# Performance work log

Hardware: AMD Instinct MI355X
Metric: run time of the kernel (lower is better)

## Reference

```python
import jax, jax.numpy as jnp
import numpy as np

VOCAB, EMB, HID = 256, 32, 128
B, T = 512, 512


def setup_inputs() -> dict:
    key = jax.random.key(0)
    ks = jax.random.split(key, 8)
    s_emb = 1.0  # torch nn.Embedding default N(0,1)
    s_lstm = 1.0 / np.sqrt(HID)  # torch LSTM uniform(-1/sqrt(H), 1/sqrt(H))
    s_cls = 1.0 / np.sqrt(HID)
    return {
        "inputs": jax.random.randint(ks[0], (B, T), 0, VOCAB, dtype=jnp.int64),
        "emb": jax.random.normal(ks[1], (VOCAB, EMB), jnp.float32) * s_emb,
        "W_ih": jax.random.uniform(ks[2], (4 * HID, EMB), jnp.float32, -s_lstm, s_lstm),
        "W_hh": jax.random.uniform(ks[3], (4 * HID, HID), jnp.float32, -s_lstm, s_lstm),
        "b_ih": jax.random.uniform(ks[4], (4 * HID,), jnp.float32, -s_lstm, s_lstm),
        "b_hh": jax.random.uniform(ks[5], (4 * HID,), jnp.float32, -s_lstm, s_lstm),
        "W_cls": jax.random.uniform(ks[6], (VOCAB, HID), jnp.float32, -s_cls, s_cls),
        "b_cls": jax.random.uniform(ks[7], (VOCAB,), jnp.float32, -s_cls, s_cls),
    }


def reference(inputs, emb, W_ih, W_hh, b_ih, b_hh, W_cls, b_cls):
    x = emb[inputs]  # [B, T, E]
    H = W_hh.shape[1]
    # Precompute input projections for all timesteps (batched GEMM): [B, T, 4H]
    xw = jnp.einsum("bte,ge->btg", x, W_ih) + b_ih + b_hh
    xw_t = jnp.transpose(xw, (1, 0, 2))  # [T, B, 4H]

    def step(carry, xw_step):
        h, c = carry
        gates = xw_step + h @ W_hh.T  # [B, 4H]
        i, f, g, o = jnp.split(gates, 4, axis=-1)  # torch gate order: i, f, g, o
        i = jax.nn.sigmoid(i)
        f = jax.nn.sigmoid(f)
        g = jnp.tanh(g)
        o = jax.nn.sigmoid(o)
        c = f * c + i * g
        h = o * jnp.tanh(c)
        return (h, c), None

    h0 = jnp.zeros((x.shape[0], H), x.dtype)
    c0 = jnp.zeros((x.shape[0], H), x.dtype)
    (h_last, _), _ = jax.lax.scan(step, (h0, c0), xw_t)
    # classifier on last hidden state: [B, vocab]
    return h_last @ W_cls.T + b_cls
```

## Files before the change

kernel.cpp:

```cpp
#include <hip/hip_runtime.h>
#include <hip/hip_bf16.h>

#define VOCAB 256
#define EMB   32
#define HID   128
#define GATES 512
#define BATCH 512
#define SEQ   512

typedef __attribute__((ext_vector_type(8))) short bf16x8;
typedef __attribute__((ext_vector_type(4))) float f32x4;

static __device__ __forceinline__ unsigned short f2bf(float f) {
  unsigned int u = __float_as_uint(f);
  return (unsigned short)((u + 0x7fffu + ((u >> 16) & 1u)) >> 16);
}

__global__ __launch_bounds__(256) void prep_kernel(
    const float* __restrict__ emb, const float* __restrict__ W_ih,
    const float* __restrict__ W_hh, const float* __restrict__ b_ih,
    const float* __restrict__ b_hh, float* __restrict__ P,
    unsigned short* __restrict__ Whh_bf) {
  const int wg  = blockIdx.x;
  const int tid = threadIdx.x;
  if (wg < VOCAB) {
    __shared__ float e[EMB];
    if (tid < EMB) e[tid] = emb[wg * EMB + tid];
    __syncthreads();
    for (int g = tid; g < GATES; g += 256) {
      float acc = b_ih[g] + b_hh[g];
      const float* w = W_ih + g * EMB;
      #pragma unroll
      for (int k = 0; k < EMB; ++k) acc += e[k] * w[k];
      P[wg * GATES + g] = acc;
    }
  } else {
    const int base = (wg - VOCAB) * 1024 + tid * 4;
    const float4 v = *(const float4*)(W_hh + base);
    ushort4 o;
    o.x = f2bf(v.x); o.y = f2bf(v.y); o.z = f2bf(v.z); o.w = f2bf(v.w);
    *(ushort4*)(Whh_bf + base) = o;
  }
}

__global__ __launch_bounds__(256, 1) void lstm_kernel(
    const int* __restrict__ inputs, const float* __restrict__ P,
    const unsigned short* __restrict__ Whh_bf,
    const float* __restrict__ W_cls, const float* __restrict__ b_cls,
    float* __restrict__ out) {
  const int wg   = blockIdx.x;
  const int tid  = threadIdx.x;
  const int wave = tid >> 6;
  const int lane = tid & 63;
  const int c16  = lane & 15;
  const int kg   = lane >> 4;
  const int b0   = wg * 2;

  const int row   = kg >> 1;
  const int jh    = kg & 1;
  const int jfull = wave * 32 + jh * 16 + c16;

  __shared__ unsigned char  chars[2][SEQ];
  __shared__ unsigned short hbuf[2][2][HID];
  __shared__ float          h_last[2][HID];

  for (int k = tid; k < 2 * SEQ; k += 256) {
    const int r = k >> 9, t = k & (SEQ - 1);
    chars[r][t] = (unsigned char)(inputs[(b0 + r) * SEQ + t] & 0xff);
  }
  ((unsigned short*)hbuf)[tid] = 0;

  bf16x8 Bfrag[8][4];
  #pragma unroll
  for (int gt = 0; gt < 4; ++gt)
    #pragma unroll
    for (int jhu = 0; jhu < 2; ++jhu) {
      const int g = gt * 128 + wave * 32 + jhu * 16 + c16;
      #pragma unroll
      for (int ks = 0; ks < 4; ++ks)
        Bfrag[gt * 2 + jhu][ks] = *(const bf16x8*)(Whh_bf + g * HID + ks * 32 + kg * 8);
    }

  const int aoff = (c16 & 1) * HID + kg * 8;
  const float* Pj = P + jfull;
  float cstate = 0.f;

  __syncthreads();

  #pragma unroll 1
  for (int t = 0; t < SEQ; ++t) {
    const int rb = t & 1;
    const int ch = chars[row][t];
    const float* Pr = Pj + ch * GATES;
    const float p0 = Pr[0];
    const float p1 = Pr[128];
    const float p2 = Pr[256];
    const float p3 = Pr[384];

    const unsigned short* hb = &hbuf[rb][0][0] + aoff;
    f32x4 acc[8] = {};
    #pragma unroll
    for (int ks = 0; ks < 4; ++ks) {
      const bf16x8 A = *(const bf16x8*)(hb + ks * 32);
      #pragma unroll
      for (int u = 0; u < 8; ++u)
        acc[u] = __builtin_amdgcn_mfma_f32_16x16x32_bf16(A, Bfrag[u][ks], acc[u], 0, 0, 0);
    }

    const float gi = jh ? (row ? acc[1][1] : acc[1][0]) : (row ? acc[0][1] : acc[0][0]);
    const float gf = jh ? (row ? acc[3][1] : acc[3][0]) : (row ? acc[2][1] : acc[2][0]);
    const float gg = jh ? (row ? acc[5][1] : acc[5][0]) : (row ? acc[4][1] : acc[4][0]);
    const float go = jh ? (row ? acc[7][1] : acc[7][0]) : (row ? acc[6][1] : acc[6][0]);

    const float ip = gi + p0;
    const float fp = gf + p1;
    const float gp = gg + p2;
    const float op = go + p3;
    const float iv = 1.f / (1.f + __expf(-ip));
    const float fv = 1.f / (1.f + __expf(-fp));
    const float gv = 1.f - 2.f / (__expf(2.f * gp) + 1.f);
    const float ov = 1.f / (1.f + __expf(-op));
    cstate = fv * cstate + iv * gv;
    const float th = 1.f - 2.f / (__expf(2.f * cstate) + 1.f);
    const float hv = ov * th;

    hbuf[rb ^ 1][row][jfull] = f2bf(hv);
    if (t == SEQ - 1) h_last[row][jfull] = hv;
    __syncthreads();
  }

  const int erow = tid >> 7;
  const int ej   = tid & 127;
  #pragma unroll
  for (int half = 0; half < 2; ++half) {
    const int v = ej + half * 128;
    float acc = b_cls[v];
    const float4* w  = (const float4*)(W_cls + v * HID);
    const float4* hh = (const float4*)&h_last[erow][0];
    #pragma unroll
    for (int k = 0; k < HID / 4; ++k) {
      const float4 wv = w[k];
      const float4 hv4 = hh[k];
      acc += wv.x * hv4.x + wv.y * hv4.y + wv.z * hv4.z + wv.w * hv4.w;
    }
    out[(b0 + erow) * VOCAB + v] = acc;
  }
}

extern "C" void kernel_launch(void* const* d_in, const int* in_sizes, int n_in,
                              void* d_out, int out_size, void* d_ws, size_t ws_size,
                              hipStream_t stream) {
  const int*   inputs = (const int*)d_in[0];
  const float* emb    = (const float*)d_in[1];
  const float* W_ih   = (const float*)d_in[2];
  const float* W_hh   = (const float*)d_in[3];
  const float* b_ih   = (const float*)d_in[4];
  const float* b_hh   = (const float*)d_in[5];
  const float* W_cls  = (const float*)d_in[6];
  const float* b_cls  = (const float*)d_in[7];
  float* outp = (float*)d_out;

  float* Ptab = (float*)d_ws;
  unsigned short* Whh_bf = (unsigned short*)((char*)d_ws + VOCAB * GATES * sizeof(float));

  prep_kernel<<<VOCAB + 64, 256, 0, stream>>>(emb, W_ih, W_hh, b_ih, b_hh, Ptab, Whh_bf);
  lstm_kernel<<<BATCH / 2, 256, 0, stream>>>(inputs, Ptab, Whh_bf, W_cls, b_cls, outp);
}
```

Measured before the change: 365.2 us.

## Use 8 waves per LSTM block and prefetch next-step input projections

Doubles the workgroup to 512 threads so each wave computes 16 hidden units (4 MFMA chains instead of 8), which shortens the serial per-step critical path of MFMA and activation work. It also software-prefetches the next timestep's gate projection rows from the P table so their global latency overlaps the current step. The cost is more waves synchronising at every step's barrier, and in the classifier each thread now handles one output.

Result: slower. 396.7 us (+8.6%).

```diff
diff --git a/kernel.cpp b/kernel.cpp
--- a/kernel.cpp
+++ b/kernel.cpp
@@ -43,7 +43,7 @@
   }
 }
 
-__global__ __launch_bounds__(256, 1) void lstm_kernel(
+__global__ __launch_bounds__(512, 2) void lstm_kernel(
     const int* __restrict__ inputs, const float* __restrict__ P,
     const unsigned short* __restrict__ Whh_bf,
     const float* __restrict__ W_cls, const float* __restrict__ b_cls,
@@ -56,30 +56,27 @@
   const int kg   = lane >> 4;
   const int b0   = wg * 2;
 
-  const int row   = kg >> 1;
-  const int jh    = kg & 1;
-  const int jfull = wave * 32 + jh * 16 + c16;
+  const int row   = kg & 1;
+  const int jfull = wave * 16 + c16;
 
   __shared__ unsigned char  chars[2][SEQ];
   __shared__ unsigned short hbuf[2][2][HID];
   __shared__ float          h_last[2][HID];
 
-  for (int k = tid; k < 2 * SEQ; k += 256) {
+  for (int k = tid; k < 2 * SEQ; k += 512) {
     const int r = k >> 9, t = k & (SEQ - 1);
     chars[r][t] = (unsigned char)(inputs[(b0 + r) * SEQ + t] & 0xff);
   }
-  ((unsigned short*)hbuf)[tid] = 0;
+  if (tid < 512) ((unsigned short*)hbuf)[tid] = 0;
 
-  bf16x8 Bfrag[8][4];
+  bf16x8 Bfrag[4][4];
   #pragma unroll
-  for (int gt = 0; gt < 4; ++gt)
+  for (int gt = 0; gt < 4; ++gt) {
+    const int g = gt * 128 + wave * 16 + c16;
     #pragma unroll
-    for (int jhu = 0; jhu < 2; ++jhu) {
-      const int g = gt * 128 + wave * 32 + jhu * 16 + c16;
-      #pragma unroll
-      for (int ks = 0; ks < 4; ++ks)
-        Bfrag[gt * 2 + jhu][ks] = *(const bf16x8*)(Whh_bf + g * HID + ks * 32 + kg * 8);
-    }
+    for (int ks = 0; ks < 4; ++ks)
+      Bfrag[gt][ks] = *(const bf16x8*)(Whh_bf + g * HID + ks * 32 + kg * 8);
+  }
 
   const int aoff = (c16 & 1) * HID + kg * 8;
   const float* Pj = P + jfull;
@@ -87,30 +84,32 @@
 
   __syncthreads();
 
+  int ch = chars[row][0];
+  const float* Pr = Pj + (size_t)ch * GATES;
+  float p0 = Pr[0], p1 = Pr[128], p2 = Pr[256], p3 = Pr[384];
+
   #pragma unroll 1
   for (int t = 0; t < SEQ; ++t) {
     const int rb = t & 1;
-    const int ch = chars[row][t];
-    const float* Pr = Pj + ch * GATES;
-    const float p0 = Pr[0];
-    const float p1 = Pr[128];
-    const float p2 = Pr[256];
-    const float p3 = Pr[384];
+
+    const int chn = chars[row][(t + 1) & (SEQ - 1)];
+    const float* Pn = Pj + (size_t)chn * GATES;
+    const float q0 = Pn[0], q1 = Pn[128], q2 = Pn[256], q3 = Pn[384];
 
     const unsigned short* hb = &hbuf[rb][0][0] + aoff;
-    f32x4 acc[8] = {};
+    f32x4 acc[4] = {};
     #pragma unroll
     for (int ks = 0; ks < 4; ++ks) {
       const bf16x8 A = *(const bf16x8*)(hb + ks * 32);
       #pragma unroll
-      for (int u = 0; u < 8; ++u)
-        acc[u] = __builtin_amdgcn_mfma_f32_16x16x32_bf16(A, Bfrag[u][ks], acc[u], 0, 0, 0);
+      for (int gt = 0; gt < 4; ++gt)
+        acc[gt] = __builtin_amdgcn_mfma_f32_16x16x32_bf16(A, Bfrag[gt][ks], acc[gt], 0, 0, 0);
     }
 
-    const float gi = jh ? (row ? acc[1][1] : acc[1][0]) : (row ? acc[0][1] : acc[0][0]);
-    const float gf = jh ? (row ? acc[3][1] : acc[3][0]) : (row ? acc[2][1] : acc[2][0]);
-    const float gg = jh ? (row ? acc[5][1] : acc[5][0]) : (row ? acc[4][1] : acc[4][0]);
-    const float go = jh ? (row ? acc[7][1] : acc[7][0]) : (row ? acc[6][1] : acc[6][0]);
+    const float gi = row ? acc[0][1] : acc[0][0];
+    const float gf = row ? acc[1][1] : acc[1][0];
+    const float gg = row ? acc[2][1] : acc[2][0];
+    const float go = row ? acc[3][1] : acc[3][0];
 
     const float ip = gi + p0;
     const float fp = gf + p1;
@@ -126,25 +125,23 @@
 
     hbuf[rb ^ 1][row][jfull] = f2bf(hv);
     if (t == SEQ - 1) h_last[row][jfull] = hv;
+
+    p0 = q0; p1 = q1; p2 = q2; p3 = q3;
     __syncthreads();
   }
 
-  const int erow = tid >> 7;
-  const int ej   = tid & 127;
+  const int erow = tid >> 8;
+  const int v    = tid & 255;
+  float acc = b_cls[v];
+  const float4* w  = (const float4*)(W_cls + v * HID);
+  const float4* hh = (const float4*)&h_last[erow][0];
   #pragma unroll
-  for (int half = 0; half < 2; ++half) {
-    const int v = ej + half * 128;
-    float acc = b_cls[v];
-    const float4* w  = (const float4*)(W_cls + v * HID);
-    const float4* hh = (const float4*)&h_last[erow][0];
-    #pragma unroll
-    for (int k = 0; k < HID / 4; ++k) {
-      const float4 wv = w[k];
-      const float4 hv4 = hh[k];
-      acc += wv.x * hv4.x + wv.y * hv4.y + wv.z * hv4.z + wv.w * hv4.w;
-    }
-    out[(b0 + erow) * VOCAB + v] = acc;
+  for (int k = 0; k < HID / 4; ++k) {
+    const float4 wv = w[k];
+    const float4 hv4 = hh[k];
+    acc += wv.x * hv4.x + wv.y * hv4.y + wv.z * hv4.z + wv.w * hv4.w;
   }
+  out[(b0 + erow) * VOCAB + v] = acc;
 }
 
 extern "C" void kernel_launch(void* const* d_in, const int* in_sizes, int n_in,
@@ -164,5 +161,5 @@
   unsigned short* Whh_bf = (unsigned short*)((char*)d_ws + VOCAB * GATES * sizeof(float));
 
   prep_kernel<<<VOCAB + 64, 256, 0, stream>>>(emb, W_ih, W_hh, b_ih, b_hh, Ptab, Whh_bf);
-  lstm_kernel<<<BATCH / 2, 256, 0, stream>>>(inputs, Ptab, Whh_bf, W_cls, b_cls, outp);
+  lstm_kernel<<<BATCH / 2, 512, 0, stream>>>(inputs, Ptab, Whh_bf, W_cls, b_cls, outp);
 }
```
